# Kernel optimization log

Measured on AMD Instinct MI355X. Metric: run time of the kernel, lower is better.

Reference implementation:

```python
import jax, jax.numpy as jnp
import numpy as np

EPS = 1e-7  # keras backend.epsilon()
NUM_ROUTING = 3


def squash(v, axis=-1):
    s2 = jnp.sum(jnp.square(v), axis=axis, keepdims=True)
    scale = s2 / (1.0 + s2) / jnp.sqrt(s2 + EPS)
    return scale * v


def setup_inputs() -> dict:
    key = jax.random.key(0)
    k1, k2 = jax.random.split(key)
    B, I, Q = 64, 2048, 16      # batch, input_num_capsule, input_dim_capsule
    J, P = 32, 32               # num_capsule, dim_capsule
    inputs = jax.random.normal(k1, (B, I, Q), dtype=jnp.float32)
    # glorot-ish scale for W: [num_capsule, input_num_capsule, dim_capsule, input_dim_capsule]
    W = jax.random.normal(k2, (J, I, P, Q), dtype=jnp.float32) * (1.0 / np.sqrt(Q))
    return {"inputs": inputs, "W": W}


def reference(inputs, W):
    # inputs_hat[b,j,i,p] = sum_q inputs[b,i,q] * W[j,i,p,q]
    hat = jnp.einsum('biq,jipq->bjip', inputs, W)
    hat_stop = jax.lax.stop_gradient(hat)
    B, J, I, P = hat.shape
    b = jnp.zeros((B, J, I), dtype=hat.dtype)
    for _ in range(NUM_ROUTING - 1):
        c = jax.nn.softmax(b, axis=1)                       # softmax over num_capsule axis
        v = squash(jnp.einsum('bji,bjip->bjp', c, hat_stop))
        b = b + jnp.einsum('bjp,bjip->bji', v, hat_stop)
    c = jax.nn.softmax(b, axis=1)
    return squash(jnp.einsum('bji,bjip->bjp', c, hat))      # [B, J, P]
```

## Files before the change

### kernel.cpp

```cpp
#include <hip/hip_runtime.h>

typedef _Float16 h8 __attribute__((ext_vector_type(8)));
typedef _Float16 h4 __attribute__((ext_vector_type(4)));
typedef float f4 __attribute__((ext_vector_type(4)));

constexpr int NB = 64;
constexpr int NI = 2048;
constexpr int NQ = 16;
constexpr int NJ = 32;
constexpr int NP = 32;
constexpr int NIP = NI / 2;
constexpr int VSZ = NB * NJ * NP;


__global__ __launch_bounds__(256)
void zero_kernel(f4* __restrict__ p)
{
    const f4 z = {0.f, 0.f, 0.f, 0.f};
    p[(size_t)blockIdx.x * 256 + threadIdx.x] = z;
}

__global__ __launch_bounds__(256)
void xpack_kernel(const float* __restrict__ X, h8* __restrict__ xp)
{
    const int ip = blockIdx.x;
    const int t = threadIdx.x;
    const int bf = t >> 6, l = t & 63;
    const int b = (l & 15) + 16 * bf;
    const int i = 2 * ip + (l >= 32 ? 1 : 0);
    const int q0 = ((l >> 4) & 1) * 8;
    const float* xs = X + ((size_t)b * NI + i) * NQ + q0;
    const float4 u = *reinterpret_cast<const float4*>(xs);
    const float4 v = *reinterpret_cast<const float4*>(xs + 4);
    h8 h;
    h[0] = (_Float16)u.x; h[1] = (_Float16)u.y; h[2] = (_Float16)u.z; h[3] = (_Float16)u.w;
    h[4] = (_Float16)v.x; h[5] = (_Float16)v.y; h[6] = (_Float16)v.z; h[7] = (_Float16)v.w;
    xp[(size_t)(ip * 4 + bf) * 64 + l] = h;
}

__global__ __launch_bounds__(256)
void wpack_kernel(const float* __restrict__ Wg, h8* __restrict__ wp)
{
    const size_t g = (size_t)blockIdx.x * 256 + threadIdx.x;
    const int l = (int)(g & 63);
    const size_t rest = g >> 6;
    const int pf = (int)(rest & 1);
    const int ip = (int)((rest >> 1) & (NIP - 1));
    const int j  = (int)(rest >> 11);
    const int i = 2 * ip + (l >= 32 ? 1 : 0);
    const int p = pf * 16 + (l & 15);
    const int q0 = ((l >> 4) & 1) * 8;
    const float* src = Wg + (((size_t)j * NI + i) * NP + p) * NQ + q0;
    const float4 u = *reinterpret_cast<const float4*>(src);
    const float4 v = *reinterpret_cast<const float4*>(src + 4);
    h8 a;
    a[0] = (_Float16)u.x; a[1] = (_Float16)u.y; a[2] = (_Float16)u.z; a[3] = (_Float16)u.w;
    a[4] = (_Float16)v.x; a[5] = (_Float16)v.y; a[6] = (_Float16)v.z; a[7] = (_Float16)v.w;
    wp[g] = a;
}

__device__ inline float sqscale(float s2)
{
    return s2 / ((1.f + s2) * sqrtf(s2 + 1e-7f));
}

template <int SMODE>
__global__ __launch_bounds__(512)
void logits_kernel(const h8* __restrict__ wp, const h8* __restrict__ xp,
                   const float* __restrict__ U1, const float* __restrict__ U2,
                   _Float16* __restrict__ cp)
{
    __shared__ float L[8][32][64];
    const int t = threadIdx.x, wv = t >> 6, l = t & 63;
    const int i0 = blockIdx.x * 8;
    const bool lo = l >= 32;
    h8 zh;
#pragma unroll
    for (int e = 0; e < 8; ++e) zh[e] = (_Float16)0.f;

#pragma unroll 1
    for (int jj = 0; jj < 4; ++jj) {
        const int j = wv * 4 + jj;

        float sreg[4][8];
#pragma unroll
        for (int bf = 0; bf < 4; ++bf) {
            const int b = (l & 15) + 16 * bf;
            const size_t base = ((size_t)b * NJ + j) * NP + (l >> 4) * 4;
            float va[8];
#pragma unroll
            for (int pf = 0; pf < 2; ++pf) {
                const f4 u = *reinterpret_cast<const f4*>(U1 + base + 16 * pf);
#pragma unroll
                for (int r = 0; r < 4; ++r) va[pf * 4 + r] = u[r] * (1.f / 32.f);
            }
            float s2 = 0.f;
#pragma unroll
            for (int e = 0; e < 8; ++e) s2 += va[e] * va[e];
            s2 += __shfl_xor(s2, 16);
            s2 += __shfl_xor(s2, 32);
            const float sc1 = sqscale(s2);
#pragma unroll
            for (int e = 0; e < 8; ++e) sreg[bf][e] = va[e] * sc1;

            if (SMODE == 1) {
                float vb[8];
#pragma unroll
                for (int pf = 0; pf < 2; ++pf) {
                    const f4 u = *reinterpret_cast<const f4*>(U2 + base + 16 * pf);
#pragma unroll
                    for (int r = 0; r < 4; ++r) vb[pf * 4 + r] = u[r];
                }
                float t2 = 0.f;
#pragma unroll
                for (int e = 0; e < 8; ++e) t2 += vb[e] * vb[e];
                t2 += __shfl_xor(t2, 16);
                t2 += __shfl_xor(t2, 32);
                const float sc2 = sqscale(t2);
#pragma unroll
                for (int e = 0; e < 8; ++e) sreg[bf][e] += vb[e] * sc2;
            }
        }

#pragma unroll 1
        for (int ipl = 0; ipl < 4; ++ipl) {
            const int ipg = blockIdx.x * 4 + ipl;
            const h8* wpji = wp + ((size_t)j * NIP + ipg) * 2 * 64 + l;
            const h8 A0 = wpji[0];
            const h8 A1 = wpji[64];
            const h8* xpb = xp + (size_t)ipg * 4 * 64 + l;
            h8 B[4];
#pragma unroll
            for (int bf = 0; bf < 4; ++bf) B[bf] = xpb[bf * 64];

#pragma unroll
            for (int half = 0; half < 2; ++half) {
                f4 D[2][4];
#pragma unroll
                for (int pf = 0; pf < 2; ++pf)
#pragma unroll
                    for (int bf = 0; bf < 4; ++bf) { f4 Z = {0.f, 0.f, 0.f, 0.f}; D[pf][bf] = Z; }
#pragma unroll
                for (int bf = 0; bf < 4; ++bf) {
                    const h8 Bm = ((half == 0) == lo) ? zh : B[bf];
                    D[0][bf] = __builtin_amdgcn_mfma_f32_16x16x32_f16(A0, Bm, D[0][bf], 0, 0, 0);
                    D[1][bf] = __builtin_amdgcn_mfma_f32_16x16x32_f16(A1, Bm, D[1][bf], 0, 0, 0);
                }
                float part[4];
#pragma unroll
                for (int bf = 0; bf < 4; ++bf) {
                    float p_ = 0.f;
#pragma unroll
                    for (int pf = 0; pf < 2; ++pf)
#pragma unroll
                        for (int r = 0; r < 4; ++r) p_ += sreg[bf][pf * 4 + r] * D[pf][bf][r];
                    p_ += __shfl_xor(p_, 16);
                    p_ += __shfl_xor(p_, 32);
                    part[bf] = p_;
                }
                const int hb = l >> 4;
                const float wval = hb == 0 ? part[0] : hb == 1 ? part[1] : hb == 2 ? part[2] : part[3];
                L[ipl * 2 + half][j][(l & 15) + 16 * hb] = wval;
            }
        }
    }
    __syncthreads();

    {
        const int b = t & 63, ii = t >> 6;
        float lv[32];
        float m = -1e30f;
#pragma unroll
        for (int j = 0; j < 32; ++j) { lv[j] = L[ii][j][b]; m = fmaxf(m, lv[j]); }
        float s = 0.f;
#pragma unroll
        for (int j = 0; j < 32; ++j) { lv[j] = __expf(lv[j] - m); s += lv[j]; }
        const float inv = 1.f / s;
#pragma unroll
        for (int j = 0; j < 32; ++j) L[ii][j][b] = lv[j] * inv;
    }
    __syncthreads();

    {
        const int jw = t >> 4, r = t & 15;
#pragma unroll 1
        for (int ii = 0; ii < 8; ++ii) {
            h4 c4;
#pragma unroll
            for (int e = 0; e < 4; ++e) c4[e] = (_Float16)L[ii][jw][16 * e + r];
            *reinterpret_cast<h4*>(cp + ((size_t)jw * NI + i0 + ii) * 64 + r * 4) = c4;
        }
    }
}

template <bool HASC>
__global__ __launch_bounds__(512)
void accum_kernel(const h8* __restrict__ wp, const h8* __restrict__ xp,
                  const _Float16* __restrict__ cp, float* __restrict__ ACC)
{
    const int t = threadIdx.x, wv = t >> 6, l = t & 63;
    const int j = blockIdx.x >> 4, is = blockIdx.x & 15;
    const bool lo = l >= 32;

    f4 D[2][4];
#pragma unroll
    for (int pf = 0; pf < 2; ++pf)
#pragma unroll
        for (int bf = 0; bf < 4; ++bf) { f4 Z = {0.f, 0.f, 0.f, 0.f}; D[pf][bf] = Z; }

    const int pbase = is * 64 + wv * 8;
#pragma unroll 1
    for (int ipl = 0; ipl < 8; ++ipl) {
        const int ipg = pbase + ipl;
        const h8* wpji = wp + ((size_t)j * NIP + ipg) * 2 * 64 + l;
        const h8 A0 = wpji[0];
        const h8 A1 = wpji[64];
        const h8* xpb = xp + (size_t)ipg * 4 * 64 + l;
        h4 c4;
        if (HASC) {
            const int i = 2 * ipg + (lo ? 1 : 0);
            c4 = *reinterpret_cast<const h4*>(cp + ((size_t)j * NI + i) * 64 + (l & 15) * 4);
        }
#pragma unroll
        for (int bf = 0; bf < 4; ++bf) {
            h8 B = xpb[bf * 64];
            if (HASC) B = B * c4[bf];
            D[0][bf] = __builtin_amdgcn_mfma_f32_16x16x32_f16(A0, B, D[0][bf], 0, 0, 0);
            D[1][bf] = __builtin_amdgcn_mfma_f32_16x16x32_f16(A1, B, D[1][bf], 0, 0, 0);
        }
    }

    __shared__ float R[8][64 * 36];
#pragma unroll
    for (int pf = 0; pf < 2; ++pf)
#pragma unroll
        for (int bf = 0; bf < 4; ++bf) {
            const int b = (l & 15) + 16 * bf, p = (l >> 4) * 4 + 16 * pf;
            *reinterpret_cast<f4*>(&R[wv][b * 36 + p]) = D[pf][bf];
        }
    __syncthreads();
#pragma unroll
    for (int k = 0; k < 4; ++k) {
        const int id = t + k * 512;
        const int b = id >> 5, p = id & 31;
        float s = 0.f;
#pragma unroll
        for (int w8 = 0; w8 < 8; ++w8) s += R[w8][b * 36 + p];
        atomicAdd(ACC + ((size_t)b * NJ + j) * NP + p, s);
    }
}

__global__ __launch_bounds__(256)
void squash_kernel(const float* __restrict__ U, float* __restrict__ OUT)
{
    const int t   = threadIdx.x;
    const int row = blockIdx.x * 8 + (t >> 5);
    const int p   = t & 31;
    const float val = U[row * 32 + p];
    float sq = val * val;
#pragma unroll
    for (int d = 1; d < 32; d <<= 1) sq += __shfl_xor(sq, d);
    OUT[row * 32 + p] = val * sqscale(sq);
}

extern "C" void kernel_launch(void* const* d_in, const int* in_sizes, int n_in,
                              void* d_out, int out_size, void* d_ws, size_t ws_size,
                              hipStream_t stream)
{
    const float* X  = (const float*)d_in[0];
    const float* Wg = (const float*)d_in[1];
    float* out = (float*)d_out;

    float* v1u = (float*)d_ws;
    float* v2u = v1u + VSZ;
    float* ou  = v2u + VSZ;
    h8* xp = (h8*)((char*)d_ws + (size_t)3 * VSZ * 4);
    _Float16* cp = (_Float16*)((char*)xp + (size_t)NIP * 4 * 64 * 16);
    h8* wpk = (h8*)((char*)cp + (size_t)NJ * NI * 64 * 2);

    xpack_kernel<<<NIP, 256, 0, stream>>>(X, xp);
    wpack_kernel<<<(NJ * NIP * 2 * 64) / 256, 256, 0, stream>>>(Wg, wpk);
    zero_kernel<<<3 * VSZ * 4 / (256 * 16), 256, 0, stream>>>((f4*)d_ws);

    accum_kernel<false><<<512, 512, 0, stream>>>(wpk, xp, nullptr, v1u);

    logits_kernel<0><<<NI / 8, 512, 0, stream>>>(wpk, xp, v1u, nullptr, cp);
    accum_kernel<true><<<512, 512, 0, stream>>>(wpk, xp, cp, v2u);

    logits_kernel<1><<<NI / 8, 512, 0, stream>>>(wpk, xp, v1u, v2u, cp);
    accum_kernel<true><<<512, 512, 0, stream>>>(wpk, xp, cp, ou);

    squash_kernel<<<VSZ / 256, 256, 0, stream>>>(ou, out);
}
```

Baseline: 145.0 us.

## Fuse W fp16 packing into first accumulation pass and prefetch next-iteration operands

Removes the separate wpack kernel and folds the fp32-to-fp16 conversion and packed-W store into the first accumulation kernel (wacc_kernel). The first routing pass therefore reads the fp32 W once and also produces the packed copy for later passes, saving one full pass over W. The accum and logits loops now software-prefetch the next iteration's A/B/c operands into registers so loads overlap the MFMAs. This costs extra registers and the fused kernel does more work per block.

```diff
diff --git a/kernel.cpp b/kernel.cpp
--- a/kernel.cpp
+++ b/kernel.cpp
@@ -38,30 +38,100 @@
     xp[(size_t)(ip * 4 + bf) * 64 + l] = h;
 }
 
-__global__ __launch_bounds__(256)
-void wpack_kernel(const float* __restrict__ Wg, h8* __restrict__ wp)
-{
-    const size_t g = (size_t)blockIdx.x * 256 + threadIdx.x;
-    const int l = (int)(g & 63);
-    const size_t rest = g >> 6;
-    const int pf = (int)(rest & 1);
-    const int ip = (int)((rest >> 1) & (NIP - 1));
-    const int j  = (int)(rest >> 11);
-    const int i = 2 * ip + (l >= 32 ? 1 : 0);
-    const int p = pf * 16 + (l & 15);
+__device__ inline float sqscale(float s2)
+{
+    return s2 / ((1.f + s2) * sqrtf(s2 + 1e-7f));
+}
+
+__global__ __launch_bounds__(512)
+void wacc_kernel(const float* __restrict__ Wg, const h8* __restrict__ xp,
+                 h8* __restrict__ wp, float* __restrict__ ACC)
+{
+    const int t = threadIdx.x, wv = t >> 6, l = t & 63;
+    const int j = blockIdx.x >> 4, is = blockIdx.x & 15;
+    const int ioff = (l >= 32) ? 1 : 0;
     const int q0 = ((l >> 4) & 1) * 8;
-    const float* src = Wg + (((size_t)j * NI + i) * NP + p) * NQ + q0;
-    const float4 u = *reinterpret_cast<const float4*>(src);
-    const float4 v = *reinterpret_cast<const float4*>(src + 4);
-    h8 a;
-    a[0] = (_Float16)u.x; a[1] = (_Float16)u.y; a[2] = (_Float16)u.z; a[3] = (_Float16)u.w;
-    a[4] = (_Float16)v.x; a[5] = (_Float16)v.y; a[6] = (_Float16)v.z; a[7] = (_Float16)v.w;
-    wp[g] = a;
-}
-
-__device__ inline float sqscale(float s2)
-{
-    return s2 / ((1.f + s2) * sqrtf(s2 + 1e-7f));
+    const int pbase = is * 64 + wv * 8;
+
+    f4 D[2][4];
+#pragma unroll
+    for (int pf = 0; pf < 2; ++pf)
+#pragma unroll
+        for (int bf = 0; bf < 4; ++bf) { f4 Z = {0.f, 0.f, 0.f, 0.f}; D[pf][bf] = Z; }
+
+    const float* wgl = Wg + ((size_t)j * NI + ioff) * (NP * NQ) + (size_t)(l & 15) * NQ + q0;
+
+    f4 u0, u1, v0, v1;
+    {
+        const float* s0 = wgl + (size_t)(2 * pbase) * (NP * NQ);
+        u0 = *reinterpret_cast<const f4*>(s0);
+        u1 = *reinterpret_cast<const f4*>(s0 + 4);
+        v0 = *reinterpret_cast<const f4*>(s0 + 16 * NQ);
+        v1 = *reinterpret_cast<const f4*>(s0 + 16 * NQ + 4);
+    }
+    h8 B0, B1, B2, B3;
+    {
+        const h8* xpb = xp + (size_t)pbase * 4 * 64 + l;
+        B0 = xpb[0]; B1 = xpb[64]; B2 = xpb[128]; B3 = xpb[192];
+    }
+
+#pragma unroll 1
+    for (int ipl = 0; ipl < 8; ++ipl) {
+        const int ipg = pbase + ipl;
+        const int nip = (ipl < 7) ? ipg + 1 : ipg;
+        f4 nu0, nu1, nv0, nv1;
+        {
+            const float* s0 = wgl + (size_t)(2 * nip) * (NP * NQ);
+            nu0 = *reinterpret_cast<const f4*>(s0);
+            nu1 = *reinterpret_cast<const f4*>(s0 + 4);
+            nv0 = *reinterpret_cast<const f4*>(s0 + 16 * NQ);
+            nv1 = *reinterpret_cast<const f4*>(s0 + 16 * NQ + 4);
+        }
+        h8 nB0, nB1, nB2, nB3;
+        {
+            const h8* xpb = xp + (size_t)nip * 4 * 64 + l;
+            nB0 = xpb[0]; nB1 = xpb[64]; nB2 = xpb[128]; nB3 = xpb[192];
+        }
+
+        h8 A0, A1;
+#pragma unroll
+        for (int e = 0; e < 4; ++e) {
+            A0[e] = (_Float16)u0[e]; A0[e + 4] = (_Float16)u1[e];
+            A1[e] = (_Float16)v0[e]; A1[e + 4] = (_Float16)v1[e];
+        }
+        const size_t wo = ((size_t)j * NIP + ipg) * 2 * 64 + l;
+        wp[wo] = A0;
+        wp[wo + 64] = A1;
+        D[0][0] = __builtin_amdgcn_mfma_f32_16x16x32_f16(A0, B0, D[0][0], 0, 0, 0);
+        D[1][0] = __builtin_amdgcn_mfma_f32_16x16x32_f16(A1, B0, D[1][0], 0, 0, 0);
+        D[0][1] = __builtin_amdgcn_mfma_f32_16x16x32_f16(A0, B1, D[0][1], 0, 0, 0);
+        D[1][1] = __builtin_amdgcn_mfma_f32_16x16x32_f16(A1, B1, D[1][1], 0, 0, 0);
+        D[0][2] = __builtin_amdgcn_mfma_f32_16x16x32_f16(A0, B2, D[0][2], 0, 0, 0);
+        D[1][2] = __builtin_amdgcn_mfma_f32_16x16x32_f16(A1, B2, D[1][2], 0, 0, 0);
+        D[0][3] = __builtin_amdgcn_mfma_f32_16x16x32_f16(A0, B3, D[0][3], 0, 0, 0);
+        D[1][3] = __builtin_amdgcn_mfma_f32_16x16x32_f16(A1, B3, D[1][3], 0, 0, 0);
+        u0 = nu0; u1 = nu1; v0 = nv0; v1 = nv1;
+        B0 = nB0; B1 = nB1; B2 = nB2; B3 = nB3;
+    }
+
+    __shared__ float R[8][64 * 36];
+#pragma unroll
+    for (int pf = 0; pf < 2; ++pf)
+#pragma unroll
+        for (int bf = 0; bf < 4; ++bf) {
+            const int b = (l & 15) + 16 * bf, p = (l >> 4) * 4 + 16 * pf;
+            *reinterpret_cast<f4*>(&R[wv][b * 36 + p]) = D[pf][bf];
+        }
+    __syncthreads();
+#pragma unroll
+    for (int k = 0; k < 4; ++k) {
+        const int id = t + k * 512;
+        const int b = id >> 5, p = id & 31;
+        float s = 0.f;
+#pragma unroll
+        for (int w8 = 0; w8 < 8; ++w8) s += R[w8][b * 36 + p];
+        atomicAdd(ACC + ((size_t)b * NJ + j) * NP + p, s);
+    }
 }
 
 template <int SMODE>
@@ -73,6 +143,7 @@
     __shared__ float L[8][32][64];
     const int t = threadIdx.x, wv = t >> 6, l = t & 63;
     const int i0 = blockIdx.x * 8;
+    const int ip0 = blockIdx.x * 4;
     const bool lo = l >= 32;
     h8 zh;
 #pragma unroll
@@ -122,12 +193,17 @@
             }
         }
 
+        const h8* wj = wp + (size_t)j * NIP * 2 * 64 + l;
+        h8 A0 = wj[(size_t)ip0 * 128];
+        h8 A1 = wj[(size_t)ip0 * 128 + 64];
+
 #pragma unroll 1
         for (int ipl = 0; ipl < 4; ++ipl) {
-            const int ipg = blockIdx.x * 4 + ipl;
-            const h8* wpji = wp + ((size_t)j * NIP + ipg) * 2 * 64 + l;
-            const h8 A0 = wpji[0];
-            const h8 A1 = wpji[64];
+            const int ipg = ip0 + ipl;
+            const int nip = (ipl < 3) ? ipg + 1 : ipg;
+            h8 nA0 = wj[(size_t)nip * 128];
+            h8 nA1 = wj[(size_t)nip * 128 + 64];
+
             const h8* xpb = xp + (size_t)ipg * 4 * 64 + l;
             h8 B[4];
 #pragma unroll
@@ -162,6 +238,7 @@
                 const float wval = hb == 0 ? part[0] : hb == 1 ? part[1] : hb == 2 ? part[2] : part[3];
                 L[ipl * 2 + half][j][(l & 15) + 16 * hb] = wval;
             }
+            A0 = nA0; A1 = nA1;
         }
     }
     __syncthreads();
@@ -193,14 +270,13 @@
     }
 }
 
-template <bool HASC>
 __global__ __launch_bounds__(512)
 void accum_kernel(const h8* __restrict__ wp, const h8* __restrict__ xp,
                   const _Float16* __restrict__ cp, float* __restrict__ ACC)
 {
     const int t = threadIdx.x, wv = t >> 6, l = t & 63;
     const int j = blockIdx.x >> 4, is = blockIdx.x & 15;
-    const bool lo = l >= 32;
+    const int ioff = (l >= 32) ? 1 : 0;
 
     f4 D[2][4];
 #pragma unroll
@@ -209,25 +285,41 @@
         for (int bf = 0; bf < 4; ++bf) { f4 Z = {0.f, 0.f, 0.f, 0.f}; D[pf][bf] = Z; }
 
     const int pbase = is * 64 + wv * 8;
+    const h8* wj = wp + (size_t)j * NIP * 2 * 64 + l;
+    const _Float16* cj = cp + ((size_t)j * NI + ioff) * 64 + (l & 15) * 4;
+
+    h8 A0 = wj[(size_t)pbase * 128];
+    h8 A1 = wj[(size_t)pbase * 128 + 64];
+    h8 B0, B1, B2, B3;
+    {
+        const h8* xpb = xp + (size_t)pbase * 4 * 64 + l;
+        B0 = xpb[0]; B1 = xpb[64]; B2 = xpb[128]; B3 = xpb[192];
+    }
+    h4 c4 = *reinterpret_cast<const h4*>(cj + (size_t)(2 * pbase) * 64);
+
 #pragma unroll 1
     for (int ipl = 0; ipl < 8; ++ipl) {
         const int ipg = pbase + ipl;
-        const h8* wpji = wp + ((size_t)j * NIP + ipg) * 2 * 64 + l;
-        const h8 A0 = wpji[0];
-        const h8 A1 = wpji[64];
-        const h8* xpb = xp + (size_t)ipg * 4 * 64 + l;
-        h4 c4;
-        if (HASC) {
-            const int i = 2 * ipg + (lo ? 1 : 0);
-            c4 = *reinterpret_cast<const h4*>(cp + ((size_t)j * NI + i) * 64 + (l & 15) * 4);
-        }
-#pragma unroll
-        for (int bf = 0; bf < 4; ++bf) {
-            h8 B = xpb[bf * 64];
-            if (HASC) B = B * c4[bf];
-            D[0][bf] = __builtin_amdgcn_mfma_f32_16x16x32_f16(A0, B, D[0][bf], 0, 0, 0);
-            D[1][bf] = __builtin_amdgcn_mfma_f32_16x16x32_f16(A1, B, D[1][bf], 0, 0, 0);
-        }
+        const int nip = (ipl < 7) ? ipg + 1 : ipg;
+        h8 nA0 = wj[(size_t)nip * 128];
+        h8 nA1 = wj[(size_t)nip * 128 + 64];
+        h8 nB0, nB1, nB2, nB3;
+        {
+            const h8* xpb = xp + (size_t)nip * 4 * 64 + l;
+            nB0 = xpb[0]; nB1 = xpb[64]; nB2 = xpb[128]; nB3 = xpb[192];
+        }
+        h4 nc4 = *reinterpret_cast<const h4*>(cj + (size_t)(2 * nip) * 64);
+
+        h8 b0 = B0 * c4[0], b1 = B1 * c4[1], b2 = B2 * c4[2], b3 = B3 * c4[3];
+        D[0][0] = __builtin_amdgcn_mfma_f32_16x16x32_f16(A0, b0, D[0][0], 0, 0, 0);
+        D[1][0] = __builtin_amdgcn_mfma_f32_16x16x32_f16(A1, b0, D[1][0], 0, 0, 0);
+        D[0][1] = __builtin_amdgcn_mfma_f32_16x16x32_f16(A0, b1, D[0][1], 0, 0, 0);
+        D[1][1] = __builtin_amdgcn_mfma_f32_16x16x32_f16(A1, b1, D[1][1], 0, 0, 0);
+        D[0][2] = __builtin_amdgcn_mfma_f32_16x16x32_f16(A0, b2, D[0][2], 0, 0, 0);
+        D[1][2] = __builtin_amdgcn_mfma_f32_16x16x32_f16(A1, b2, D[1][2], 0, 0, 0);
+        D[0][3] = __builtin_amdgcn_mfma_f32_16x16x32_f16(A0, b3, D[0][3], 0, 0, 0);
+        D[1][3] = __builtin_amdgcn_mfma_f32_16x16x32_f16(A1, b3, D[1][3], 0, 0, 0);
+        A0 = nA0; A1 = nA1; B0 = nB0; B1 = nB1; B2 = nB2; B3 = nB3; c4 = nc4;
     }
 
     __shared__ float R[8][64 * 36];
@@ -279,16 +371,15 @@
     h8* wpk = (h8*)((char*)cp + (size_t)NJ * NI * 64 * 2);
 
     xpack_kernel<<<NIP, 256, 0, stream>>>(X, xp);
-    wpack_kernel<<<(NJ * NIP * 2 * 64) / 256, 256, 0, stream>>>(Wg, wpk);
     zero_kernel<<<3 * VSZ * 4 / (256 * 16), 256, 0, stream>>>((f4*)d_ws);
 
-    accum_kernel<false><<<512, 512, 0, stream>>>(wpk, xp, nullptr, v1u);
+    wacc_kernel<<<512, 512, 0, stream>>>(Wg, xp, wpk, v1u);
 
     logits_kernel<0><<<NI / 8, 512, 0, stream>>>(wpk, xp, v1u, nullptr, cp);
-    accum_kernel<true><<<512, 512, 0, stream>>>(wpk, xp, cp, v2u);
+    accum_kernel<<<512, 512, 0, stream>>>(wpk, xp, cp, v2u);
 
     logits_kernel<1><<<NI / 8, 512, 0, stream>>>(wpk, xp, v1u, v2u, cp);
-    accum_kernel<true><<<512, 512, 0, stream>>>(wpk, xp, cp, ou);
+    accum_kernel<<<512, 512, 0, stream>>>(wpk, xp, cp, ou);
 
     squash_kernel<<<VSZ / 256, 256, 0, stream>>>(ou, out);
 }
```

New measurement: 139.9 us. 1.04x faster.
